# Kernel tuning notes

Hardware: AMD Instinct MI355X
Metric: run time of the kernel (lower is better)

The kernel has to match this reference:

```python
import jax, jax.numpy as jnp
import numpy as np

N_INPUT = 4096
N_NEURONS = 4096
T = 500
DT = 1.0
RATE = 0.05  # Bernoulli input spike probability per timestep

# LIF constants (Diehl&Cook-style excitatory / inhibitory populations)
E_REST, E_RESET, E_THRESH, E_TAU, E_REFRAC = -65.0, -65.0, -52.0, 100.0, 5.0
I_REST, I_RESET, I_THRESH, I_TAU, I_REFRAC = -60.0, -45.0, -40.0, 10.0, 2.0


def setup_inputs() -> dict:
    key = jax.random.key(0)
    k1, k2 = jax.random.split(key, 2)
    # Input group spike train: [T, n_input] of {0,1} floats (Poisson-like)
    inpts_X = (jax.random.uniform(k1, (T, N_INPUT)) < RATE).astype(jnp.float32)
    # X -> Ae learned weights (positive, small)
    w_xe = jax.random.uniform(k2, (N_INPUT, N_NEURONS), dtype=jnp.float32) * 0.3
    eye = jnp.eye(N_NEURONS, dtype=jnp.float32)
    # Ae -> Ai: one-to-one excitation; Ai -> Ae: all-but-self inhibition
    w_ei = 22.5 * eye
    w_ie = -17.5 * (1.0 - eye)
    return {"inpts_X": inpts_X, "w_xe": w_xe, "w_ei": w_ei, "w_ie": w_ie, "time": T}


def _lif(v, rc, inpt, rest, reset, thresh, tau, refrac):
    # Integrate only outside refractory period
    active = (rc <= 0).astype(v.dtype)
    v = v + (DT / tau) * (rest - v) + active * inpt
    rc = jnp.maximum(rc - DT, 0.0)
    s = (v >= thresh).astype(v.dtype)
    rc = jnp.where(s > 0, refrac, rc)
    v = jnp.where(s > 0, reset, v)
    return v, rc, s


def reference(inpts_X, w_xe, w_ei, w_ie, time):
    n_x = inpts_X.shape[1]
    n_e = w_xe.shape[1]
    n_i = w_ei.shape[1]
    f32 = inpts_X.dtype

    def step(carry, x_t):
        s_x, v_e, rc_e, s_e, v_i, rc_i, s_i = carry
        # get_inputs(): messages use spikes from the END of the previous step
        in_e = s_x @ w_xe + s_i @ w_ie   # inputs to excitatory group
        in_i = s_e @ w_ei                # inputs to inhibitory group
        s_x_new = x_t                    # InputGroup: s = current input row
        v_e2, rc_e2, s_e2 = _lif(v_e, rc_e, in_e, E_REST, E_RESET, E_THRESH, E_TAU, E_REFRAC)
        v_i2, rc_i2, s_i2 = _lif(v_i, rc_i, in_i, I_REST, I_RESET, I_THRESH, I_TAU, I_REFRAC)
        new_carry = (s_x_new, v_e2, rc_e2, s_e2, v_i2, rc_i2, s_i2)
        return new_carry, (s_x_new, s_e2, s_i2)

    init = (
        jnp.zeros((n_x,), f32),
        jnp.full((n_e,), E_REST, f32), jnp.zeros((n_e,), f32), jnp.zeros((n_e,), f32),
        jnp.full((n_i,), I_REST, f32), jnp.zeros((n_i,), f32), jnp.zeros((n_i,), f32),
    )
    _, (sx, se, si) = jax.lax.scan(step, init, inpts_X[: int(time)])
    # spikes dict -> concatenated [T, n_x + n_e + n_i]
    return jnp.concatenate([sx, se, si], axis=1)
```

## Files before the change

kernel.cpp:

```cpp
#include <hip/hip_runtime.h>

#define N 4096
#define OUTW 12288

__global__ void compact_spikes(const float* __restrict__ X, int* __restrict__ idx,
                               int* __restrict__ cnt, float* __restrict__ out, int T) {
    int t = blockIdx.x;
    const float* row = X + (size_t)t * N;
    __shared__ int counts[256];
    int tid = threadIdx.x;
    int base = tid * 16;
    float4 r0 = *(const float4*)(row + base);
    float4 r1 = *(const float4*)(row + base + 4);
    float4 r2 = *(const float4*)(row + base + 8);
    float4 r3 = *(const float4*)(row + base + 12);
    float* orow = out + (size_t)t * OUTW + base;
    *(float4*)(orow)      = r0;
    *(float4*)(orow + 4)  = r1;
    *(float4*)(orow + 8)  = r2;
    *(float4*)(orow + 12) = r3;
    float vals[16];
    *(float4*)(vals)      = r0;
    *(float4*)(vals + 4)  = r1;
    *(float4*)(vals + 8)  = r2;
    *(float4*)(vals + 12) = r3;
    int ks[16];
    int c = 0;
    #pragma unroll
    for (int q = 0; q < 16; ++q) {
        if (vals[q] != 0.0f) ks[c++] = base + q;
    }
    counts[tid] = c;
    __syncthreads();
    int off = 0;
    for (int i = 0; i < tid; ++i) off += counts[i];
    int* op = idx + (size_t)t * N;
    for (int q = 0; q < c; ++q) op[off + q] = ks[q];
    if (tid == 255) cnt[t] = off + c;
}

__global__ void gather_xw(const float* __restrict__ W, const int* __restrict__ idx,
                          const int* __restrict__ cnt, float* __restrict__ XW) {
    int b = blockIdx.x;
    int t = b >> 2;
    int tile = b & 3;
    int col = tile * 1024 + threadIdx.x * 4;
    float4 acc = {0.f, 0.f, 0.f, 0.f};
    if (t > 0) {
        int r = t - 1;
        int c = cnt[r];
        const int* ip = idx + (size_t)r * N;
        __shared__ int sidx[4096];
        for (int s = threadIdx.x; s < c; s += blockDim.x) sidx[s] = ip[s];
        __syncthreads();
        int s = 0;
        for (; s + 4 <= c; s += 4) {
            int k0 = sidx[s], k1 = sidx[s + 1], k2 = sidx[s + 2], k3 = sidx[s + 3];
            float4 w0 = *(const float4*)(W + (size_t)k0 * N + col);
            float4 w1 = *(const float4*)(W + (size_t)k1 * N + col);
            float4 w2 = *(const float4*)(W + (size_t)k2 * N + col);
            float4 w3 = *(const float4*)(W + (size_t)k3 * N + col);
            acc.x += w0.x; acc.y += w0.y; acc.z += w0.z; acc.w += w0.w;
            acc.x += w1.x; acc.y += w1.y; acc.z += w1.z; acc.w += w1.w;
            acc.x += w2.x; acc.y += w2.y; acc.z += w2.z; acc.w += w2.w;
            acc.x += w3.x; acc.y += w3.y; acc.z += w3.z; acc.w += w3.w;
        }
        for (; s < c; ++s) {
            int k = sidx[s];
            float4 w0 = *(const float4*)(W + (size_t)k * N + col);
            acc.x += w0.x; acc.y += w0.y; acc.z += w0.z; acc.w += w0.w;
        }
    }
    *(float4*)(XW + (size_t)t * N + col) = acc;
}

__global__ void __launch_bounds__(1024)
recurrent(const float* __restrict__ XW, unsigned char* __restrict__ pk, int T) {
    const int tid = threadIdx.x;
    const int lane = tid & 63;
    __shared__ unsigned int cS[3];
    if (tid < 3) cS[tid] = 0u;

    float ve[4], ref[4], si_f[4];
    unsigned int R = 0u, E = 0u;
    #pragma unroll
    for (int q = 0; q < 4; ++q) { ve[q] = -65.0f; ref[q] = 0.0f; si_f[q] = 0.0f; }

    const float4* xwp = (const float4*)XW + tid;
    float4 xw = xwp[0];
    unsigned char* pkp = pk + tid;
    __syncthreads();

    int t = 0;
    #define STEP(PAR)                                                          \
    {                                                                          \
        unsigned int Sint = cS[(PAR + 2) % 3];     \
        float4 xw_n = xw;                                                      \
        if (t + 1 < T) xw_n = xwp[(size_t)(t + 1) * 1024];                     \
        if (tid == 0) cS[(PAR + 1) % 3] = 0u;        \
                         \
        unsigned int nz = (R | (R >> 1)) & 0x01010101u;                        \
        unsigned int z  = (nz ^ 0x01010101u) & E;                              \
        R = (R - nz) | (z << 1);                                               \
        int c0 = __popcll(__ballot((z & 0x000000ffu) != 0u));                  \
        int c1 = __popcll(__ballot((z & 0x0000ff00u) != 0u));                  \
        int c2 = __popcll(__ballot((z & 0x00ff0000u) != 0u));                  \
        int c3 = __popcll(__ballot((z & 0xff000000u) != 0u));                  \
        if (lane == 0) atomicAdd(&cS[PAR], (unsigned int)(c0 + c1 + c2 + c3)); \
                              \
        float Sf = (float)Sint;                                                \
        const float xq[4] = {xw.x, xw.y, xw.z, xw.w};                          \
        int sb[4];                                                             \
        _Pragma("unroll")                                                      \
        for (int q = 0; q < 4; ++q) {                                          \
            float dS = Sf - si_f[q];                       \
            float in_e = xq[q] - 17.5f * dS;               \
            float in_sel = (ref[q] <= 0.0f) ? in_e : 0.0f;                     \
            float v = ve[q] + 0.01f * (-65.0f - ve[q]) + in_sel;               \
            float rc = fmaxf(ref[q] - 1.0f, 0.0f);                             \
            int s = (v >= -52.0f) ? 1 : 0;                                     \
            ref[q] = s ? 5.0f : rc;                                            \
            ve[q]  = s ? -65.0f : v;                                           \
            sb[q] = s;                                                         \
        }                                                                      \
        unsigned int sbits = (unsigned int)sb[0] | ((unsigned int)sb[1] << 1) |\
                             ((unsigned int)sb[2] << 2) |                      \
                             ((unsigned int)sb[3] << 3);                       \
        E = (sbits * 0x00204081u) & 0x01010101u;        \
        unsigned int znib = (z * 0x10204080u) >> 24;    \
        if (t < T) pkp[(size_t)t * 1024] = (unsigned char)(sbits | znib);      \
        si_f[0] = (float)(z & 1u);                                             \
        si_f[1] = (float)((z >> 8) & 1u);                                      \
        si_f[2] = (float)((z >> 16) & 1u);                                     \
        si_f[3] = (float)((z >> 24) & 1u);                                     \
        xw = xw_n;                                                             \
        __syncthreads();                                                       \
        ++t;                                                                   \
    }

    for (int u = 0; u < 167; ++u) {
        STEP(0)
        STEP(1)
        STEP(2)
    }
    #undef STEP
}

__global__ void expand(const unsigned char* __restrict__ pk, float* __restrict__ out, int T) {
    int i = blockIdx.x * 256 + threadIdx.x;
    if (i >= T * 1024) return;
    int t = i >> 10;
    int g = i & 1023;
    unsigned int b = pk[i];
    float* orow = out + (size_t)t * OUTW + N + (size_t)g * 4;
    float4 se4 = {(float)(b & 1u), (float)((b >> 1) & 1u),
                  (float)((b >> 2) & 1u), (float)((b >> 3) & 1u)};
    float4 si4 = {(float)((b >> 4) & 1u), (float)((b >> 5) & 1u),
                  (float)((b >> 6) & 1u), (float)((b >> 7) & 1u)};
    *(float4*)orow = se4;
    *(float4*)(orow + N) = si4;
}

extern "C" void kernel_launch(void* const* d_in, const int* in_sizes, int n_in,
                              void* d_out, int out_size, void* d_ws, size_t ws_size,
                              hipStream_t stream) {
    const float* X   = (const float*)d_in[0];
    const float* Wxe = (const float*)d_in[1];
    int T = in_sizes[0] / N;
    float* out = (float*)d_out;

    float* XW = (float*)d_ws;
    int* idx  = (int*)((char*)d_ws + (size_t)T * N * 4);
    int* cnt  = (int*)((char*)d_ws + (size_t)2 * T * N * 4);
    unsigned char* pk = (unsigned char*)idx;

    compact_spikes<<<T, 256, 0, stream>>>(X, idx, cnt, out, T);
    gather_xw<<<T * 4, 256, 0, stream>>>(Wxe, idx, cnt, XW);
    recurrent<<<1, 1024, 0, stream>>>(XW, pk, T);
    expand<<<(T * 1024 + 255) / 256, 256, 0, stream>>>(pk, out, T);
}
```

Measured before the change: 460.0 us.

## Shrink recurrent block to 256 threads with 16 neurons per thread

The single-block serial recurrent kernel now runs 256 threads, each handling 16 neurons instead of 4. This cuts the number of wavefronts that must meet at every per-timestep barrier and atomic. The ballot-and-popcount spike counting is replaced by a byte-sum plus a wavefront shuffle reduction. Each thread writes one 32-bit packed word per step, laid out so the existing expand kernel still decodes it. In exchange, each thread does four times the serial work per step and needs more registers.

```diff
diff --git a/kernel.cpp b/kernel.cpp
--- a/kernel.cpp
+++ b/kernel.cpp
@@ -74,45 +74,63 @@
     *(float4*)(XW + (size_t)t * N + col) = acc;
 }
 
-__global__ void __launch_bounds__(1024)
+__global__ void __launch_bounds__(256)
 recurrent(const float* __restrict__ XW, unsigned char* __restrict__ pk, int T) {
     const int tid = threadIdx.x;
     const int lane = tid & 63;
     __shared__ unsigned int cS[3];
     if (tid < 3) cS[tid] = 0u;
 
-    float ve[4], ref[4], si_f[4];
-    unsigned int R = 0u, E = 0u;
+    float ve[16], ref[16], si_f[16];
+    unsigned int R[4] = {0u, 0u, 0u, 0u};
+    unsigned int E[4] = {0u, 0u, 0u, 0u};
     #pragma unroll
-    for (int q = 0; q < 4; ++q) { ve[q] = -65.0f; ref[q] = 0.0f; si_f[q] = 0.0f; }
-
-    const float4* xwp = (const float4*)XW + tid;
-    float4 xw = xwp[0];
-    unsigned char* pkp = pk + tid;
+    for (int q = 0; q < 16; ++q) { ve[q] = -65.0f; ref[q] = 0.0f; si_f[q] = 0.0f; }
+
+    const float4* xwp = (const float4*)XW + (size_t)tid * 4;
+    float4 xw0 = xwp[0], xw1 = xwp[1], xw2 = xwp[2], xw3 = xwp[3];
+    unsigned int* pk32 = (unsigned int*)pk + tid;
     __syncthreads();
 
     int t = 0;
     #define STEP(PAR)                                                          \
     {                                                                          \
         unsigned int Sint = cS[(PAR + 2) % 3];     \
-        float4 xw_n = xw;                                                      \
-        if (t + 1 < T) xw_n = xwp[(size_t)(t + 1) * 1024];                     \
+        float4 n0 = xw0, n1 = xw1, n2 = xw2, n3 = xw3;                         \
+        if (t + 1 < T) {                                                       \
+            const float4* p = xwp + (size_t)(t + 1) * 1024;                    \
+            n0 = p[0]; n1 = p[1]; n2 = p[2]; n3 = p[3];                        \
+        }                                                                      \
         if (tid == 0) cS[(PAR + 1) % 3] = 0u;        \
                          \
-        unsigned int nz = (R | (R >> 1)) & 0x01010101u;                        \
-        unsigned int z  = (nz ^ 0x01010101u) & E;                              \
-        R = (R - nz) | (z << 1);                                               \
-        int c0 = __popcll(__ballot((z & 0x000000ffu) != 0u));                  \
-        int c1 = __popcll(__ballot((z & 0x0000ff00u) != 0u));                  \
-        int c2 = __popcll(__ballot((z & 0x00ff0000u) != 0u));                  \
-        int c3 = __popcll(__ballot((z & 0xff000000u) != 0u));                  \
-        if (lane == 0) atomicAdd(&cS[PAR], (unsigned int)(c0 + c1 + c2 + c3)); \
-                              \
+        unsigned int z[4];                                                     \
+        _Pragma("unroll")                                                      \
+        for (int g = 0; g < 4; ++g) {                                          \
+            unsigned int nz = (R[g] | (R[g] >> 1)) & 0x01010101u;              \
+            unsigned int zg = (nz ^ 0x01010101u) & E[g];                       \
+            R[g] = (R[g] - nz) | (zg << 1);                                    \
+            z[g] = zg;                                                         \
+        }                                                                      \
+                        \
+        unsigned int zsum = (z[0] + z[1]) + (z[2] + z[3]);                     \
+        int tot = (int)((zsum * 0x01010101u) >> 24);                           \
+        tot += __shfl_xor(tot, 1, 64);                                         \
+        tot += __shfl_xor(tot, 2, 64);                                         \
+        tot += __shfl_xor(tot, 4, 64);                                         \
+        tot += __shfl_xor(tot, 8, 64);                                         \
+        tot += __shfl_xor(tot, 16, 64);                                        \
+        tot += __shfl_xor(tot, 32, 64);                                        \
+        if (lane == 0) atomicAdd(&cS[PAR], (unsigned int)tot);                 \
+                           \
         float Sf = (float)Sint;                                                \
-        const float xq[4] = {xw.x, xw.y, xw.z, xw.w};                          \
-        int sb[4];                                                             \
-        _Pragma("unroll")                                                      \
-        for (int q = 0; q < 4; ++q) {                                          \
+        float xq[16];                                                          \
+        *(float4*)(xq)      = xw0;                                             \
+        *(float4*)(xq + 4)  = xw1;                                             \
+        *(float4*)(xq + 8)  = xw2;                                             \
+        *(float4*)(xq + 12) = xw3;                                             \
+        unsigned int sbits = 0u;                                               \
+        _Pragma("unroll")                                                      \
+        for (int q = 0; q < 16; ++q) {                                         \
             float dS = Sf - si_f[q];                       \
             float in_e = xq[q] - 17.5f * dS;               \
             float in_sel = (ref[q] <= 0.0f) ? in_e : 0.0f;                     \
@@ -121,19 +139,26 @@
             int s = (v >= -52.0f) ? 1 : 0;                                     \
             ref[q] = s ? 5.0f : rc;                                            \
             ve[q]  = s ? -65.0f : v;                                           \
-            sb[q] = s;                                                         \
+            sbits |= (unsigned int)s << q;                                     \
         }                                                                      \
-        unsigned int sbits = (unsigned int)sb[0] | ((unsigned int)sb[1] << 1) |\
-                             ((unsigned int)sb[2] << 2) |                      \
-                             ((unsigned int)sb[3] << 3);                       \
-        E = (sbits * 0x00204081u) & 0x01010101u;        \
-        unsigned int znib = (z * 0x10204080u) >> 24;    \
-        if (t < T) pkp[(size_t)t * 1024] = (unsigned char)(sbits | znib);      \
-        si_f[0] = (float)(z & 1u);                                             \
-        si_f[1] = (float)((z >> 8) & 1u);                                      \
-        si_f[2] = (float)((z >> 16) & 1u);                                     \
-        si_f[3] = (float)((z >> 24) & 1u);                                     \
-        xw = xw_n;                                                             \
+                   \
+        _Pragma("unroll")                                                      \
+        for (int g = 0; g < 4; ++g)                                            \
+            E[g] = (((sbits >> (4 * g)) & 0xFu) * 0x00204081u) & 0x01010101u;  \
+                                                       \
+        _Pragma("unroll")                                                      \
+        for (int q = 0; q < 16; ++q)                                           \
+            si_f[q] = (float)((z[q >> 2] >> ((q & 3) * 8)) & 1u);              \
+                \
+        unsigned int xsp = sbits;                                              \
+        xsp = (xsp | (xsp << 8)) & 0x00FF00FFu;                                \
+        xsp = (xsp | (xsp << 4)) & 0x0F0F0F0Fu;     \
+        unsigned int w = xsp;                                                  \
+        _Pragma("unroll")                                                      \
+        for (int g = 0; g < 4; ++g)                                            \
+            w |= ((z[g] * 0x10204080u) >> 24) << (8 * g);    \
+        if (t < T) pk32[(size_t)t * 256] = w;                                  \
+        xw0 = n0; xw1 = n1; xw2 = n2; xw3 = n3;                                \
         __syncthreads();                                                       \
         ++t;                                                                   \
     }
@@ -176,6 +201,6 @@
 
     compact_spikes<<<T, 256, 0, stream>>>(X, idx, cnt, out, T);
     gather_xw<<<T * 4, 256, 0, stream>>>(Wxe, idx, cnt, XW);
-    recurrent<<<1, 1024, 0, stream>>>(XW, pk, T);
+    recurrent<<<1, 256, 0, stream>>>(XW, pk, T);
     expand<<<(T * 1024 + 255) / 256, 256, 0, stream>>>(pk, out, T);
 }
```

After: 605.3 us. 1.32x slower.
